# Optimization experiments

Measured on AMD Instinct MI355X. Metric: run time of the kernel, lower is better.

Reference implementation:

```python
import jax, jax.numpy as jnp
import numpy as np

N_NODES = 50000
N_EDGES = 800000
IN_DIM = 128
OUT_DIM = 128
NEG_INIT = -1e9  # matches torch fill_(-1e9) init for scatter amax
LEAKY_SLOPE = 0.01  # nn.LeakyReLU default


def setup_inputs() -> dict:
    key = jax.random.key(0)
    ks = jax.random.split(key, 8)
    x = jax.random.normal(ks[0], (N_NODES, IN_DIM), dtype=jnp.float32)
    edge_index = jax.random.randint(ks[1], (2, N_EDGES), 0, N_NODES, dtype=jnp.int64)
    edge_weight = jax.random.uniform(ks[2], (N_EDGES,), dtype=jnp.float32)
    # MLP params (nn.Linear default init: U(-1/sqrt(fan_in), 1/sqrt(fan_in)))
    s1 = 1.0 / np.sqrt(IN_DIM)
    s2 = 1.0 / np.sqrt(OUT_DIM)
    w1 = jax.random.uniform(ks[3], (OUT_DIM, IN_DIM), minval=-s1, maxval=s1, dtype=jnp.float32)
    b1 = jax.random.uniform(ks[4], (OUT_DIM,), minval=-s1, maxval=s1, dtype=jnp.float32)
    w2 = jax.random.uniform(ks[5], (OUT_DIM, OUT_DIM), minval=-s2, maxval=s2, dtype=jnp.float32)
    b2 = jax.random.uniform(ks[6], (OUT_DIM,), minval=-s2, maxval=s2, dtype=jnp.float32)
    eps = jnp.zeros((1,), dtype=jnp.float32)
    return {"x": x, "edge_index": edge_index, "edge_weight": edge_weight,
            "w1": w1, "b1": b1, "w2": w2, "b2": b2, "eps": eps}


def reference(x, edge_index, edge_weight, w1, b1, w2, b2, eps):
    src = edge_index[0]
    dst = edge_index[1]
    # gather + optional edge-weight scale: [E, D]
    messages = x[src] * edge_weight[:, None]
    # scatter-max to dst; init at -1e9 so include_self=False semantics hold
    agg = jnp.full(x.shape, NEG_INIT, dtype=x.dtype).at[dst].max(messages)
    agg = jnp.where(agg == NEG_INIT, jnp.zeros_like(agg), agg)  # isolated nodes -> 0
    h = (1.0 + eps) * x + agg  # eps broadcasts ([1])
    h = h @ w1.T + b1
    h = jnp.where(h >= 0, h, LEAKY_SLOPE * h)  # LeakyReLU
    out = h @ w2.T + b2
    return out
```

## Files before the change

### kernel.cpp

```cpp
#include <hip/hip_runtime.h>
#include <stdint.h>

#define NN 50000
#define NE 800000
#define D  128
#define CAP 64
#define OVF_CAP 131072

#define CNT_OFF     64
#define OVF_CNT_OFF (CNT_OFF + NN)
#define OVF_OFF     (OVF_CNT_OFF + 4)
#define BKT_OFF     312320
#define XH_OFF      (BKT_OFF + NN * CAP)
#define WH_OFF      (XH_OFF + 65536 * (D / 2))

#define HSTRIDE 136
#define SLOTS   24
#define WLDS    (SLOTS * 256 + 1024)

#define FILL_BLKS 3125
#define PX_BLKS   6250
#define PW_BLKS   32

typedef _Float16 half8 __attribute__((ext_vector_type(8)));
typedef __attribute__((ext_vector_type(4))) float float4v;

__device__ __forceinline__ float b2f(uint16_t u) {
    union { uint32_t u; float f; } v; v.u = ((uint32_t)u) << 16; return v.f;
}
__device__ __forceinline__ uint16_t f2b(float f) {
    union { float f; uint32_t u; } v; v.f = f;
    uint32_t r = v.u + 0x7fffu + ((v.u >> 16) & 1u);
    return (uint16_t)(r >> 16);
}
__device__ __forceinline__ ushort f2h(float f) {
    union { _Float16 h; ushort u; } v; v.h = (_Float16)f; return v.u;
}
__device__ __forceinline__ float h2f(ushort u) {
    union { ushort u; _Float16 h; } v; v.u = u; return (float)v.h;
}

__device__ __forceinline__ void gload_lds16(const void* g, void* l) {
    __builtin_amdgcn_global_load_lds(
        (const __attribute__((address_space(1))) void*)g,
        (__attribute__((address_space(3))) void*)l, 16, 0, 0);
}

__device__ __forceinline__ void block_probe(const uint16_t* __restrict__ xraw,
                                            const int* __restrict__ eraw,
                                            int* sflags) {
    int t = threadIdx.x;
    if (t < 64) {
        float v0 = b2f(xraw[2 * t]);
        float v1 = b2f(xraw[2 * t + 1]);
        int bad = (!(v0 > -1e4f && v0 < 1e4f)) || (!(v1 > -1e4f && v1 < 1e4f));
        unsigned long long bm = __ballot(bad);
        int nz = (t < 32) ? (eraw[2 * t + 1] != 0) : 0;
        unsigned long long im = __ballot(nz);
        if (t == 0) { sflags[0] = bm ? 1 : 0; sflags[1] = im ? 0 : 1; }
    }
    __syncthreads();
}

__global__ __launch_bounds__(256) void prep_fill_kernel(
    const uint16_t* __restrict__ xraw,
    const int*      __restrict__ eraw,
    const uint16_t* __restrict__ ewraw,
    const uint16_t* __restrict__ w1raw,
    const uint16_t* __restrict__ w2raw,
    int* __restrict__ ws)
{
    __shared__ int sflags[2];
    block_probe(xraw, eraw, sflags);
    const int f32 = sflags[0], i64 = sflags[1];

    int bid = blockIdx.x;
    if (bid < FILL_BLKS) {
        int e = bid * 256 + threadIdx.x;
        int src, dst;
        if (i64) {
            const long long* e64 = (const long long*)eraw;
            src = (int)e64[e];
            dst = (int)e64[NE + e];
        } else {
            src = eraw[e];
            dst = eraw[NE + e];
        }
        if ((unsigned)src >= NN || (unsigned)dst >= NN) return;
        uint w = f32 ? (uint)f2h(((const float*)ewraw)[e]) : (uint)f2h(b2f(ewraw[e]));
        uint entry = (w << 16) | (uint)src;
        int slot = atomicAdd(ws + CNT_OFF + dst, 1) + 1;
        if (slot < CAP) {
            ((uint*)(ws + BKT_OFF))[(size_t)dst * CAP + slot] = entry;
        } else {
            int o = atomicAdd(ws + OVF_CNT_OFF, 1) + 1;
            if (o < OVF_CAP) {
                ws[OVF_OFF + 2 * o]     = dst;
                ws[OVF_OFF + 2 * o + 1] = (int)entry;
            }
        }
    } else if (bid < FILL_BLKS + PX_BLKS) {
        int i4 = ((bid - FILL_BLKS) * 256 + threadIdx.x) * 4;
        ushort* dst = (ushort*)(ws + XH_OFF);
        if (f32) {
            float4 v = *(const float4*)((const float*)xraw + i4);
            ushort4 o; o.x = f2h(v.x); o.y = f2h(v.y); o.z = f2h(v.z); o.w = f2h(v.w);
            *(ushort4*)(dst + i4) = o;
        } else {
            ushort4 v = *(const ushort4*)(xraw + i4);
            ushort4 o; o.x = f2h(b2f(v.x)); o.y = f2h(b2f(v.y));
            o.z = f2h(b2f(v.z)); o.w = f2h(b2f(v.w));
            *(ushort4*)(dst + i4) = o;
        }
    } else {
        int i4 = ((bid - FILL_BLKS - PX_BLKS) * 256 + threadIdx.x) * 4;
        const uint16_t* src = (i4 < 16384) ? w1raw : w2raw;
        int off = i4 & 16383;
        ushort* dst = (ushort*)(ws + WH_OFF);
        if (f32) {
            float4 v = *(const float4*)((const float*)src + off);
            ushort4 o; o.x = f2h(v.x); o.y = f2h(v.y); o.z = f2h(v.z); o.w = f2h(v.w);
            *(ushort4*)(dst + i4) = o;
        } else {
            ushort4 v = *(const ushort4*)(src + off);
            ushort4 o; o.x = f2h(b2f(v.x)); o.y = f2h(b2f(v.y));
            o.z = f2h(b2f(v.z)); o.w = f2h(b2f(v.w));
            *(ushort4*)(dst + i4) = o;
        }
    }
}

__global__ __launch_bounds__(256, 4) void gmlp_kernel(
    const uint16_t* __restrict__ xraw,
    const int*      __restrict__ eraw,
    const uint16_t* __restrict__ b1raw,
    const uint16_t* __restrict__ b2raw,
    const uint16_t* __restrict__ epsraw,
    const int* __restrict__ ws,
    uint16_t* __restrict__ outraw)
{
    __shared__ char smem[4][WLDS];
    __shared__ uint tl[16 * (HSTRIDE / 2)];
    __shared__ int  sflags[2];
    ushort* hl = (ushort*)&smem[0][0];

    const int tid  = threadIdx.x;
    const int wave = tid >> 6;
    const int lane = tid & 63;
    const int m    = lane & 15;
    const int quad = lane >> 4;
    const int node0 = blockIdx.x * 16;

    const ushort* w1h = (const ushort*)(ws + WH_OFF);
    const ushort* w2h = w1h + 16384;
    const uint*   xh  = (const uint*)(ws + XH_OFF);
    const char*   xhb = (const char*)xh;
    const uint*   bkt = (const uint*)(ws + BKT_OFF);
    const uint    lane4 = (uint)lane * 4;
    const uint    sub16 = (uint)(lane & 15) * 16;
    char*         wbuf  = smem[wave];

    gload_lds16((const char*)(bkt + (size_t)(node0 + wave * 4) * CAP) + (uint)lane * 16,
                wbuf + SLOTS * 256);

    int deg[4];
    uint xv[4];
    #pragma unroll
    for (int j = 0; j < 4; ++j) {
        deg[j] = ws[CNT_OFF + node0 + wave * 4 + j] + 1;
        xv[j]  = xh[(size_t)(node0 + wave * 4 + j) * 64 + lane];
    }

    block_probe(xraw, eraw, sflags);
    const int f32 = sflags[0];
    const float eps1 = 1.0f + (f32 ? ((const float*)epsraw)[0] : b2f(epsraw[0]));

    asm volatile("s_waitcnt vmcnt(0)" ::: "memory");

    #pragma unroll
    for (int j = 0; j < 4; ++j) {
        int nl = wave * 4 + j;
        int n  = node0 + nl;
        int cnt = (deg[j] < CAP) ? deg[j] : CAP;
        const uint* ewp = (const uint*)(wbuf + SLOTS * 256 + j * 256);

        asm volatile("s_waitcnt lgkmcnt(0)" ::: "memory");

        #pragma unroll
        for (int g = 0; g < SLOTS / 4; ++g) {
            uint slot = (uint)(g * 4) + (uint)(lane >> 4);
            uint e0 = ewp[slot];
            e0 = (slot < (uint)cnt) ? e0 : 0xffffffffu;
            gload_lds16(xhb + ((e0 & 0xffffu) << 8) + sub16, wbuf + g * 1024);
        }

        uint mm[4] = {~0u, ~0u, ~0u, ~0u};

        asm volatile("s_waitcnt vmcnt(3)" ::: "memory");
        #pragma unroll
        for (int g = 0; g < 3; ++g) {
            uint4 e4 = *(const uint4*)(ewp + g * 4);
            #pragma unroll
            for (int t = 0; t < 4; ++t) {
                int u = g * 4 + t;
                uint e0 = (u < cnt) ? ((const uint*)&e4)[t] : 0xffffffffu;
                uint v = *(const uint*)(wbuf + u * 256 + lane4);
                uint p;
                asm("v_pk_mul_f16 %0, %1, %2 op_sel:[0,1] op_sel_hi:[1,1]"
                    : "=v"(p) : "v"(v), "v"(e0));
                asm("v_pk_max_f16 %0, %0, %1" : "+v"(mm[u & 3]) : "v"(p));
            }
        }
        asm volatile("s_waitcnt vmcnt(0)" ::: "memory");
        #pragma unroll
        for (int g = 3; g < SLOTS / 4; ++g) {
            uint4 e4 = *(const uint4*)(ewp + g * 4);
            #pragma unroll
            for (int t = 0; t < 4; ++t) {
                int u = g * 4 + t;
                uint e0 = (u < cnt) ? ((const uint*)&e4)[t] : 0xffffffffu;
                uint v = *(const uint*)(wbuf + u * 256 + lane4);
                uint p;
                asm("v_pk_mul_f16 %0, %1, %2 op_sel:[0,1] op_sel_hi:[1,1]"
                    : "=v"(p) : "v"(v), "v"(e0));
                asm("v_pk_max_f16 %0, %0, %1" : "+v"(mm[u & 3]) : "v"(p));
            }
        }
        for (int i = SLOTS; i < cnt; ++i) {
            uint e0 = ewp[i];
            uint v  = *(const uint*)(xhb + ((e0 & 0xffffu) << 8) + lane4);
            uint p;
            asm("v_pk_mul_f16 %0, %1, %2 op_sel:[0,1] op_sel_hi:[1,1]"
                : "=v"(p) : "v"(v), "v"(e0));
            asm("v_pk_max_f16 %0, %0, %1" : "+v"(mm[0]) : "v"(p));
        }

        asm("v_pk_max_f16 %0, %0, %1" : "+v"(mm[0]) : "v"(mm[1]));
        asm("v_pk_max_f16 %0, %0, %1" : "+v"(mm[2]) : "v"(mm[3]));
        asm("v_pk_max_f16 %0, %0, %1" : "+v"(mm[0]) : "v"(mm[2]));
        float mx = h2f((ushort)(mm[0] & 0xffffu));
        float my = h2f((ushort)(mm[0] >> 16));

        if (deg[j] > CAP) {
            int novf = ws[OVF_CNT_OFF] + 1;
            if (novf > OVF_CAP) novf = OVF_CAP;
            for (int o = 0; o < novf; ++o) {
                if (ws[OVF_OFF + 2 * o] == n) {
                    uint e0 = (uint)ws[OVF_OFF + 2 * o + 1];
                    uint v  = xh[(e0 & 0xffffu) * 64 + lane];
                    float w = h2f((ushort)(e0 >> 16));
                    mx = fmaxf(mx, h2f((ushort)(v & 0xffffu)) * w);
                    my = fmaxf(my, h2f((ushort)(v >> 16)) * w);
                }
            }
        }
        if (deg[j] == 0) { mx = 0.f; my = 0.f; }

        float t0 = eps1 * h2f((ushort)(xv[j] & 0xffffu)) + mx;
        float t1 = eps1 * h2f((ushort)(xv[j] >> 16)) + my;
        tl[nl * (HSTRIDE / 2) + lane] = (uint)f2h(t0) | ((uint)f2h(t1) << 16);
    }
    __syncthreads();

    half8 a[4];
    {
        const ushort* arow = (const ushort*)tl + m * HSTRIDE + quad * 8;
        #pragma unroll
        for (int kb = 0; kb < 4; ++kb) a[kb] = *(const half8*)(arow + kb * 32);
    }

    #pragma unroll
    for (int t = 0; t < 2; ++t) {
        int ct = wave * 2 + t;
        float4v c = {0.f, 0.f, 0.f, 0.f};
        const ushort* brow = w1h + (size_t)(ct * 16 + m) * 128 + quad * 8;
        #pragma unroll
        for (int kb = 0; kb < 4; ++kb)
            c = __builtin_amdgcn_mfma_f32_16x16x32_f16(a[kb], *(const half8*)(brow + kb * 32), c, 0, 0, 0);
        float bias = f32 ? ((const float*)b1raw)[ct * 16 + m] : b2f(b1raw[ct * 16 + m]);
        #pragma unroll
        for (int r = 0; r < 4; ++r) {
            float v = c[r] + bias;
            v = (v >= 0.f) ? v : 0.01f * v;
            hl[(quad * 4 + r) * HSTRIDE + ct * 16 + m] = f2h(v);
        }
    }
    __syncthreads();

    half8 ah[4];
    {
        const ushort* hrow = hl + m * HSTRIDE + quad * 8;
        #pragma unroll
        for (int kb = 0; kb < 4; ++kb) ah[kb] = *(const half8*)(hrow + kb * 32);
    }

    #pragma unroll
    for (int t = 0; t < 2; ++t) {
        int ct = wave * 2 + t;
        float4v c = {0.f, 0.f, 0.f, 0.f};
        const ushort* brow = w2h + (size_t)(ct * 16 + m) * 128 + quad * 8;
        #pragma unroll
        for (int kb = 0; kb < 4; ++kb)
            c = __builtin_amdgcn_mfma_f32_16x16x32_f16(ah[kb], *(const half8*)(brow + kb * 32), c, 0, 0, 0);
        float bias = f32 ? ((const float*)b2raw)[ct * 16 + m] : b2f(b2raw[ct * 16 + m]);
        #pragma unroll
        for (int r = 0; r < 4; ++r) {
            float v = c[r] + bias;
            size_t o = (size_t)(node0 + quad * 4 + r) * 128 + ct * 16 + m;
            if (f32) ((float*)outraw)[o] = v;
            else     outraw[o] = f2b(v);
        }
    }
}

extern "C" void kernel_launch(void* const* d_in, const int* in_sizes, int n_in,
                              void* d_out, int out_size, void* d_ws, size_t ws_size,
                              hipStream_t stream) {
    const uint16_t* x    = (const uint16_t*)d_in[0];
    const int*      eidx = (const int*)     d_in[1];
    const uint16_t* ew   = (const uint16_t*)d_in[2];
    const uint16_t* w1   = (const uint16_t*)d_in[3];
    const uint16_t* b1   = (const uint16_t*)d_in[4];
    const uint16_t* w2   = (const uint16_t*)d_in[5];
    const uint16_t* b2   = (const uint16_t*)d_in[6];
    const uint16_t* eps  = (const uint16_t*)d_in[7];
    uint16_t*       out  = (uint16_t*)d_out;
    int* ws = (int*)d_ws;

    hipMemsetAsync((char*)d_ws + (size_t)CNT_OFF * 4, 0xFF,
                   (size_t)(NN + 1) * 4, stream);
    prep_fill_kernel<<<FILL_BLKS + PX_BLKS + PW_BLKS, 256, 0, stream>>>(
        x, eidx, ew, w1, w2, ws);
    gmlp_kernel<<<NN / 16, 256, 0, stream>>>(x, eidx, b1, b2, eps, ws, out);
}
```

Before: 206.1 us.

## Partition edge buckets per XCD to keep fill atomics local

The edge-bucket fill now keeps a separate counter and 10-slot bucket per XCD for each destination node, using workgroup-scope relaxed atomics. The aim is to avoid cross-die coherence traffic on the global per-node counters. The gather kernel merges the eight sub-buckets with a wave prefix sum over the counts and handles degrees above CAP through an extra pass. In exchange it adds an 8x larger counter memset, scattered bucket reads, and extra merge logic. Correctness depends on every atomic to a given sub-counter coming from the same XCD, since the atomics are workgroup-scoped.

```diff
diff --git a/kernel.cpp b/kernel.cpp
--- a/kernel.cpp
+++ b/kernel.cpp
@@ -5,14 +5,16 @@
 #define NE 800000
 #define D  128
 #define CAP 64
-#define OVF_CAP 131072
-
-#define CNT_OFF     64
-#define OVF_CNT_OFF (CNT_OFF + NN)
+#define SCAP 10
+#define NXCD 8
+#define OVF_CAP 65536
+
+#define CNT8_OFF    64
+#define OVF_CNT_OFF (CNT8_OFF + NXCD * NN)
 #define OVF_OFF     (OVF_CNT_OFF + 4)
-#define BKT_OFF     312320
-#define XH_OFF      (BKT_OFF + NN * CAP)
-#define WH_OFF      (XH_OFF + 65536 * (D / 2))
+#define BKT8_OFF    531200
+#define XH_OFF      (BKT8_OFF + NXCD * NN * SCAP)
+#define WH_OFF      (XH_OFF + (NN + 1) * (D / 2))
 
 #define HSTRIDE 136
 #define SLOTS   24
@@ -76,6 +78,10 @@
 
     int bid = blockIdx.x;
     if (bid < FILL_BLKS) {
+        uint xcd;
+        asm volatile("s_getreg_b32 %0, hwreg(HW_REG_XCC_ID)" : "=s"(xcd));
+        xcd &= (NXCD - 1);
+
         int e = bid * 256 + threadIdx.x;
         int src, dst;
         if (i64) {
@@ -89,9 +95,10 @@
         if ((unsigned)src >= NN || (unsigned)dst >= NN) return;
         uint w = f32 ? (uint)f2h(((const float*)ewraw)[e]) : (uint)f2h(b2f(ewraw[e]));
         uint entry = (w << 16) | (uint)src;
-        int slot = atomicAdd(ws + CNT_OFF + dst, 1) + 1;
-        if (slot < CAP) {
-            ((uint*)(ws + BKT_OFF))[(size_t)dst * CAP + slot] = entry;
+        int slot = __hip_atomic_fetch_add(ws + CNT8_OFF + (size_t)xcd * NN + dst, 1,
+                                          __ATOMIC_RELAXED, __HIP_MEMORY_SCOPE_WORKGROUP) + 1;
+        if (slot < SCAP) {
+            ((uint*)(ws + BKT8_OFF))[((size_t)xcd * NN + dst) * SCAP + slot] = entry;
         } else {
             int o = atomicAdd(ws + OVF_CNT_OFF, 1) + 1;
             if (o < OVF_CAP) {
@@ -155,34 +162,56 @@
     const ushort* w2h = w1h + 16384;
     const uint*   xh  = (const uint*)(ws + XH_OFF);
     const char*   xhb = (const char*)xh;
-    const uint*   bkt = (const uint*)(ws + BKT_OFF);
+    const uint*   bkt8 = (const uint*)(ws + BKT8_OFF);
     const uint    lane4 = (uint)lane * 4;
     const uint    sub16 = (uint)(lane & 15) * 16;
     char*         wbuf  = smem[wave];
-
-    gload_lds16((const char*)(bkt + (size_t)(node0 + wave * 4) * CAP) + (uint)lane * 16,
-                wbuf + SLOTS * 256);
-
-    int deg[4];
+    uint*         ebw   = (uint*)(wbuf + SLOTS * 256);
+
+    int total[4], ecnt[4]; bool ovfl[4];
+    #pragma unroll
+    for (int j = 0; j < 4; ++j) {
+        int n = node0 + wave * 4 + j;
+        int raw = 0;
+        if (lane < 8) raw = ws[CNT8_OFF + lane * NN + n] + 1;
+        int ck = (raw < SCAP) ? raw : SCAP;
+        int inc = ck;
+        #pragma unroll
+        for (int d = 1; d < 8; d <<= 1) {
+            int v = __shfl_up(inc, d);
+            if (lane >= d) inc += v;
+        }
+        int tot = __shfl(inc, 7);
+        total[j] = tot;
+        ecnt[j]  = (tot < CAP) ? tot : CAP;
+        ovfl[j]  = (__ballot(lane < 8 && raw > SCAP) != 0ull);
+        int kk = 0, off = 0, prev = 0;
+        #pragma unroll
+        for (int k2 = 0; k2 < 8; ++k2) {
+            int ik = __shfl(inc, k2);
+            if (lane >= prev && lane < ik) { kk = k2; off = lane - prev; }
+            prev = ik;
+        }
+        uint e = 0xffffffffu;
+        if (lane < ecnt[j]) e = bkt8[((size_t)kk * NN + n) * SCAP + off];
+        ebw[j * 64 + lane] = e;
+    }
+
     uint xv[4];
     #pragma unroll
-    for (int j = 0; j < 4; ++j) {
-        deg[j] = ws[CNT_OFF + node0 + wave * 4 + j] + 1;
-        xv[j]  = xh[(size_t)(node0 + wave * 4 + j) * 64 + lane];
-    }
+    for (int j = 0; j < 4; ++j)
+        xv[j] = xh[(size_t)(node0 + wave * 4 + j) * 64 + lane];
 
     block_probe(xraw, eraw, sflags);
     const int f32 = sflags[0];
     const float eps1 = 1.0f + (f32 ? ((const float*)epsraw)[0] : b2f(epsraw[0]));
 
-    asm volatile("s_waitcnt vmcnt(0)" ::: "memory");
-
     #pragma unroll
     for (int j = 0; j < 4; ++j) {
         int nl = wave * 4 + j;
         int n  = node0 + nl;
-        int cnt = (deg[j] < CAP) ? deg[j] : CAP;
-        const uint* ewp = (const uint*)(wbuf + SLOTS * 256 + j * 256);
+        int cnt = ecnt[j];
+        const uint* ewp = ebw + j * 64;
 
         asm volatile("s_waitcnt lgkmcnt(0)" ::: "memory");
 
@@ -191,7 +220,9 @@
             uint slot = (uint)(g * 4) + (uint)(lane >> 4);
             uint e0 = ewp[slot];
             e0 = (slot < (uint)cnt) ? e0 : 0xffffffffu;
-            gload_lds16(xhb + ((e0 & 0xffffu) << 8) + sub16, wbuf + g * 1024);
+            uint row = e0 & 0xffffu;
+            row = (row < NN) ? row : NN;
+            gload_lds16(xhb + ((size_t)row << 8) + sub16, wbuf + g * 1024);
         }
 
         uint mm[4] = {~0u, ~0u, ~0u, ~0u};
@@ -228,11 +259,29 @@
         }
         for (int i = SLOTS; i < cnt; ++i) {
             uint e0 = ewp[i];
-            uint v  = *(const uint*)(xhb + ((e0 & 0xffffu) << 8) + lane4);
+            uint v  = *(const uint*)(xhb + ((size_t)(e0 & 0xffffu) << 8) + lane4);
             uint p;
             asm("v_pk_mul_f16 %0, %1, %2 op_sel:[0,1] op_sel_hi:[1,1]"
                 : "=v"(p) : "v"(v), "v"(e0));
             asm("v_pk_max_f16 %0, %0, %1" : "+v"(mm[0]) : "v"(p));
+        }
+        if (total[j] > CAP) {
+            int idx = 0;
+            for (int k2 = 0; k2 < 8; ++k2) {
+                int raw2 = ws[CNT8_OFF + k2 * NN + n] + 1;
+                int c2 = (raw2 < SCAP) ? raw2 : SCAP;
+                for (int o2 = 0; o2 < c2; ++o2) {
+                    if (idx >= CAP) {
+                        uint e0 = bkt8[((size_t)k2 * NN + n) * SCAP + o2];
+                        uint v  = *(const uint*)(xhb + ((size_t)(e0 & 0xffffu) << 8) + lane4);
+                        uint p;
+                        asm("v_pk_mul_f16 %0, %1, %2 op_sel:[0,1] op_sel_hi:[1,1]"
+                            : "=v"(p) : "v"(v), "v"(e0));
+                        asm("v_pk_max_f16 %0, %0, %1" : "+v"(mm[0]) : "v"(p));
+                    }
+                    ++idx;
+                }
+            }
         }
 
         asm("v_pk_max_f16 %0, %0, %1" : "+v"(mm[0]) : "v"(mm[1]));
@@ -241,20 +290,20 @@
         float mx = h2f((ushort)(mm[0] & 0xffffu));
         float my = h2f((ushort)(mm[0] >> 16));
 
-        if (deg[j] > CAP) {
+        if (ovfl[j]) {
             int novf = ws[OVF_CNT_OFF] + 1;
             if (novf > OVF_CAP) novf = OVF_CAP;
             for (int o = 0; o < novf; ++o) {
                 if (ws[OVF_OFF + 2 * o] == n) {
                     uint e0 = (uint)ws[OVF_OFF + 2 * o + 1];
-                    uint v  = xh[(e0 & 0xffffu) * 64 + lane];
+                    uint v  = xh[(size_t)(e0 & 0xffffu) * 64 + lane];
                     float w = h2f((ushort)(e0 >> 16));
                     mx = fmaxf(mx, h2f((ushort)(v & 0xffffu)) * w);
                     my = fmaxf(my, h2f((ushort)(v >> 16)) * w);
                 }
             }
         }
-        if (deg[j] == 0) { mx = 0.f; my = 0.f; }
+        if (total[j] == 0) { mx = 0.f; my = 0.f; }
 
         float t0 = eps1 * h2f((ushort)(xv[j] & 0xffffu)) + mx;
         float t1 = eps1 * h2f((ushort)(xv[j] >> 16)) + my;
@@ -327,8 +376,8 @@
     uint16_t*       out  = (uint16_t*)d_out;
     int* ws = (int*)d_ws;
 
-    hipMemsetAsync((char*)d_ws + (size_t)CNT_OFF * 4, 0xFF,
-                   (size_t)(NN + 1) * 4, stream);
+    hipMemsetAsync((char*)d_ws + (size_t)CNT8_OFF * 4, 0xFF,
+                   ((size_t)NXCD * NN + 1) * 4, stream);
     prep_fill_kernel<<<FILL_BLKS + PX_BLKS + PW_BLKS, 256, 0, stream>>>(
         x, eidx, ew, w1, w2, ws);
     gmlp_kernel<<<NN / 16, 256, 0, stream>>>(x, eidx, b1, b2, eps, ws, out);
```

Result: faster. 198.1 us (-3.9%).
